# Performance work log

Measured on AMD Instinct MI355X. Metric: run time of the kernel, lower is better.

The kernel has to match this reference:

```python
import jax, jax.numpy as jnp
import numpy as np

B, F, W, H, D = 128, 1024, 32, 64, 64  # batch, n_features, window_size, hidden_state, output_dim


def setup_inputs() -> dict:
    key = jax.random.key(0)
    ks = jax.random.split(key, 8)
    sd = 0.05
    return {
        "x": jax.random.normal(ks[0], (B, F, W), jnp.float32),
        # dense_state: Dense(output_dim) on concat([cell, hidden]) -> [2H, D]
        "W_state": jax.random.normal(ks[1], (2 * H, D), jnp.float32) * sd,
        "b_state": jnp.zeros((D,), jnp.float32),
        # dense: Dense(output_dim, use_bias=False) on input last dim W -> [W, D]
        "W_in": jax.random.normal(ks[2], (W, D), jnp.float32) * sd,
        # Dense(1) scoring layer (shared; original re-creates it each call)
        "w_attn": jax.random.normal(ks[3], (D, 1), jnp.float32) * sd,
        "b_attn": jnp.zeros((1,), jnp.float32),
        # Keras LSTMCell params, gate order i, f, g(c~), o
        "Wx": jax.random.normal(ks[4], (F, 4 * H), jnp.float32) * sd,
        "Wh": jax.random.normal(ks[5], (H, 4 * H), jnp.float32) * sd,
        "b_lstm": jnp.zeros((4 * H,), jnp.float32),
    }


def _forward(x, W_state, b_state, W_in, w_attn, b_attn, Wx, Wh, b_lstm):
    b, f, w = x.shape
    h_dim = Wh.shape[0]
    # dense(input) is loop-invariant: [B, F, D]
    dense_in = jnp.einsum('bfw,wd->bfd', x, W_in)
    xs = jnp.moveaxis(x, 2, 0)  # [W, B, F]: per-timestep slices input[:, :, i]
    h0 = jnp.zeros((b, h_dim), x.dtype)
    c0 = jnp.zeros((b, h_dim), x.dtype)

    def step(carry, x_t):
        h, c = carry
        # original unpacks `s, h = state` with state=[h,c], so it concats [cell, hidden]
        attn_in = jnp.concatenate([c, h], axis=1)             # [B, 2H]
        z = jnp.tanh(attn_in @ W_state + b_state)[:, None, :] + dense_in  # [B, F, D]
        presoft = z @ w_attn + b_attn                         # [B, F, 1]
        # faithful: softmax over last (size-1) axis -> all ones
        alpha = jax.nn.softmax(presoft, axis=-1)
        x_tilde = alpha[..., 0] * x_t                         # [B, F]
        gates = x_tilde @ Wx + h @ Wh + b_lstm                # [B, 4H]
        i_g, f_g, g_g, o_g = jnp.split(gates, 4, axis=1)
        c_new = jax.nn.sigmoid(f_g) * c + jax.nn.sigmoid(i_g) * jnp.tanh(g_g)
        h_new = jax.nn.sigmoid(o_g) * jnp.tanh(c_new)
        # original appends state[1] == CELL state (due to the s,h swap)
        return (h_new, c_new), c_new

    _, outs = jax.lax.scan(step, (h0, c0), xs)                # [W, B, H]
    return jnp.transpose(outs, (1, 0, 2))                     # [B, W, H]


def reference(x, W_state, b_state, W_in, w_attn, b_attn, Wx, Wh, b_lstm):
    return _forward(x, W_state, b_state, W_in, w_attn, b_attn, Wx, Wh, b_lstm)
```

## Files before the change

### kernel.cpp

```cpp
#include <hip/hip_runtime.h>
#include <math.h>

#define B_   128
#define F_   1024
#define W_   32
#define H_   64
#define K4H  256

__global__ __launch_bounds__(256) void gates_gemm(
    const float* __restrict__ x,
    const float* __restrict__ Wx,
    float* __restrict__ G) {
  __shared__ float As[32][64];
  __shared__ float Bs[32][64];

  const int tid   = threadIdx.x;
  const int tm    = tid & 15;
  const int tn    = tid >> 4;
  const int mtile = blockIdx.x;
  const int ntile = blockIdx.y;
  const int b0    = mtile * 2;

  float acc[4][4];
#pragma unroll
  for (int i = 0; i < 4; ++i)
#pragma unroll
    for (int j = 0; j < 4; ++j) acc[i][j] = 0.f;

  for (int f0 = 0; f0 < F_; f0 += 32) {
#pragma unroll
    for (int i = 0; i < 2; ++i) {
      int l  = tid + i * 256;
      int t0 = (l & 7) * 4;
      int fl = (l >> 3) & 31;
      int bl = l >> 8;
      float4 v = *(const float4*)&x[(((size_t)(b0 + bl)) * F_ + (f0 + fl)) * W_ + t0];
      *(float4*)&As[fl][bl * 32 + t0] = v;
    }
#pragma unroll
    for (int i = 0; i < 2; ++i) {
      int l  = tid + i * 256;
      int n0 = (l & 15) * 4;
      int fl = l >> 4;
      float4 v = *(const float4*)&Wx[(size_t)(f0 + fl) * K4H + ntile * 64 + n0];
      *(float4*)&Bs[fl][n0] = v;
    }
    __syncthreads();

#pragma unroll
    for (int f = 0; f < 32; ++f) {
      float4 a4 = *(const float4*)&As[f][tm * 4];
      float4 b4 = *(const float4*)&Bs[f][tn * 4];
      float av[4] = {a4.x, a4.y, a4.z, a4.w};
      float bv[4] = {b4.x, b4.y, b4.z, b4.w};
#pragma unroll
      for (int i = 0; i < 4; ++i)
#pragma unroll
        for (int j = 0; j < 4; ++j)
          acc[i][j] = fmaf(av[i], bv[j], acc[i][j]);
    }
    __syncthreads();
  }

#pragma unroll
  for (int i = 0; i < 4; ++i) {
    int m = mtile * 64 + tm * 4 + i;
    int k = ntile * 64 + tn * 4;
    float4 v = make_float4(acc[i][0], acc[i][1], acc[i][2], acc[i][3]);
    *(float4*)&G[(size_t)m * K4H + k] = v;
  }
}

__device__ __forceinline__ float fast_sigmoid(float v) {
  return 1.f / (1.f + __expf(-v));
}
__device__ __forceinline__ float fast_tanh(float v) {
  return 1.f - 2.f / (__expf(2.f * v) + 1.f);
}

__global__ __launch_bounds__(256) void lstm_seq(
    const float* __restrict__ G,
    const float* __restrict__ Wh,
    const float* __restrict__ bl,
    float* __restrict__ out) {
  __shared__ float sh[H_];
  __shared__ float sact[K4H];

  const int b = blockIdx.x;
  const int k = threadIdx.x;

  float wcol[H_];
#pragma unroll
  for (int j = 0; j < H_; ++j) wcol[j] = Wh[j * K4H + k];
  const float bias = bl[k];

  float c = 0.f;
  if (k < H_) sh[k] = 0.f;
  __syncthreads();

  const float* Gb = G + (size_t)b * W_ * K4H;
  float* outb = out + (size_t)b * W_ * H_;

  for (int t = 0; t < W_; ++t) {
    float g = Gb[t * K4H + k] + bias;
#pragma unroll
    for (int j = 0; j < H_; ++j) g = fmaf(sh[j], wcol[j], g);

    float act;
    if (k < 2 * H_ || k >= 3 * H_) {
      act = fast_sigmoid(g);
    } else {
      act = fast_tanh(g);
    }
    sact[k] = act;
    __syncthreads();

    if (k < H_) {
      float ig = sact[k];
      float fg = sact[H_ + k];
      float gg = sact[2 * H_ + k];
      float og = sact[3 * H_ + k];
      c = fg * c + ig * gg;
      sh[k] = og * fast_tanh(c);
      outb[t * H_ + k] = c;
    }
    __syncthreads();
  }
}

extern "C" void kernel_launch(void* const* d_in, const int* in_sizes, int n_in,
                              void* d_out, int out_size, void* d_ws, size_t ws_size,
                              hipStream_t stream) {
  const float* x      = (const float*)d_in[0];
  const float* Wx     = (const float*)d_in[6];
  const float* Wh     = (const float*)d_in[7];
  const float* b_lstm = (const float*)d_in[8];
  float* out = (float*)d_out;
  float* G   = (float*)d_ws;

  dim3 g1(64, 4);
  gates_gemm<<<g1, dim3(256), 0, stream>>>(x, Wx, G);
  lstm_seq<<<dim3(B_), dim3(256), 0, stream>>>(G, Wh, b_lstm, out);
}
```

Baseline: 147.0 us.

## Use split-bf16 MFMA GEMM with split-K and a register-broadcast LSTM recurrence

```diff
diff --git a/kernel.cpp b/kernel.cpp
--- a/kernel.cpp
+++ b/kernel.cpp
@@ -6,125 +6,221 @@
 #define W_   32
 #define H_   64
 #define K4H  256
-
-__global__ __launch_bounds__(256) void gates_gemm(
+#define M_   (B_ * W_)
+#define K2_  (2 * F_)
+
+typedef __attribute__((ext_vector_type(8))) short  short8;
+typedef __attribute__((ext_vector_type(4))) float  f32x4;
+
+__device__ __forceinline__ unsigned bf16_rne(float v) {
+  unsigned u = __float_as_uint(v);
+  return (u + 0x7FFFu + ((u >> 16) & 1u)) >> 16;
+}
+__device__ __forceinline__ unsigned pack_hilo(float v) {
+  unsigned hi = bf16_rne(v);
+  float    hf = __uint_as_float(hi << 16);
+  unsigned lo = bf16_rne(v - hf);
+  return hi | (lo << 16);
+}
+
+__global__ __launch_bounds__(256) void conv_w(const float* __restrict__ Wx,
+                                              unsigned* __restrict__ B2) {
+  __shared__ unsigned T[256][17];
+  const int tid = threadIdx.x;
+  const int f0  = blockIdx.x * 16;
+#pragma unroll
+  for (int i = 0; i < 4; ++i) {
+    int l = tid + i * 256;
+    int n0 = (l & 63) * 4;
+    int fl = l >> 6;
+    float4 v = *(const float4*)&Wx[(size_t)(f0 + fl) * K4H + n0];
+    T[n0 + 0][fl] = pack_hilo(v.x);
+    T[n0 + 1][fl] = pack_hilo(v.y);
+    T[n0 + 2][fl] = pack_hilo(v.z);
+    T[n0 + 3][fl] = pack_hilo(v.w);
+  }
+  __syncthreads();
+#pragma unroll
+  for (int i = 0; i < 4; ++i) {
+    int l  = tid + i * 256;
+    int c4 = (l & 3) * 4;
+    int n  = l >> 2;
+    uint4 o;
+    o.x = T[n][c4 + 0]; o.y = T[n][c4 + 1]; o.z = T[n][c4 + 2]; o.w = T[n][c4 + 3];
+    *(uint4*)&B2[(size_t)n * (K2_ / 2) + f0 + c4] = o;
+  }
+}
+
+__global__ __launch_bounds__(256) void gemm_mfma(
     const float* __restrict__ x,
-    const float* __restrict__ Wx,
-    float* __restrict__ G) {
-  __shared__ float As[32][64];
-  __shared__ float Bs[32][64];
-
+    const unsigned* __restrict__ B2,
+    float* __restrict__ Gp, int S) {
+  __shared__ unsigned lA[128 * 36];
+  __shared__ unsigned lB[128 * 36];
   const int tid   = threadIdx.x;
-  const int tm    = tid & 15;
-  const int tn    = tid >> 4;
   const int mtile = blockIdx.x;
   const int ntile = blockIdx.y;
-  const int b0    = mtile * 2;
-
-  float acc[4][4];
-#pragma unroll
-  for (int i = 0; i < 4; ++i)
-#pragma unroll
-    for (int j = 0; j < 4; ++j) acc[i][j] = 0.f;
-
-  for (int f0 = 0; f0 < F_; f0 += 32) {
-#pragma unroll
-    for (int i = 0; i < 2; ++i) {
+  const int s     = blockIdx.z;
+  const int NIT   = 32 / S;
+  const int wv = tid >> 6, lane = tid & 63;
+  const int wm = wv & 1, wn = wv >> 1;
+  const int lm = lane & 15, q = lane >> 4;
+
+  f32x4 acc[4][4];
+#pragma unroll
+  for (int a = 0; a < 4; ++a)
+#pragma unroll
+    for (int bb = 0; bb < 4; ++bb) acc[a][bb] = (f32x4){0.f, 0.f, 0.f, 0.f};
+
+  const int b0 = mtile * 4;
+  float4 ax[4];
+  uint4  bxr[4];
+
+  auto prefetch = [&](int iter) {
+    const int f0 = (s * NIT + iter) * 32;
+#pragma unroll
+    for (int i = 0; i < 4; ++i) {
       int l  = tid + i * 256;
       int t0 = (l & 7) * 4;
       int fl = (l >> 3) & 31;
       int bl = l >> 8;
-      float4 v = *(const float4*)&x[(((size_t)(b0 + bl)) * F_ + (f0 + fl)) * W_ + t0];
-      *(float4*)&As[fl][bl * 32 + t0] = v;
-    }
-#pragma unroll
-    for (int i = 0; i < 2; ++i) {
+      ax[i] = *(const float4*)&x[(((size_t)(b0 + bl)) * F_ + (f0 + fl)) * W_ + t0];
+    }
+#pragma unroll
+    for (int i = 0; i < 4; ++i) {
+      int l   = tid + i * 256;
+      int c16 = l & 7;
+      int nl  = l >> 3;
+      bxr[i] = *(const uint4*)&B2[(size_t)(ntile * 128 + nl) * (K2_ / 2) + f0 + c16 * 4];
+    }
+  };
+
+  prefetch(0);
+  for (int iter = 0; iter < NIT; ++iter) {
+    __syncthreads();
+#pragma unroll
+    for (int i = 0; i < 4; ++i) {
       int l  = tid + i * 256;
-      int n0 = (l & 15) * 4;
-      int fl = l >> 4;
-      float4 v = *(const float4*)&Wx[(size_t)(f0 + fl) * K4H + ntile * 64 + n0];
-      *(float4*)&Bs[fl][n0] = v;
+      int t0 = (l & 7) * 4;
+      int fl = (l >> 3) & 31;
+      int bl = l >> 8;
+      int m  = bl * 32 + t0;
+      lA[(m + 0) * 36 + fl] = pack_hilo(ax[i].x);
+      lA[(m + 1) * 36 + fl] = pack_hilo(ax[i].y);
+      lA[(m + 2) * 36 + fl] = pack_hilo(ax[i].z);
+      lA[(m + 3) * 36 + fl] = pack_hilo(ax[i].w);
+    }
+#pragma unroll
+    for (int i = 0; i < 4; ++i) {
+      int l   = tid + i * 256;
+      int c16 = l & 7;
+      int nl  = l >> 3;
+      *(uint4*)&lB[nl * 36 + c16 * 4] = bxr[i];
     }
     __syncthreads();
-
-#pragma unroll
-    for (int f = 0; f < 32; ++f) {
-      float4 a4 = *(const float4*)&As[f][tm * 4];
-      float4 b4 = *(const float4*)&Bs[f][tn * 4];
-      float av[4] = {a4.x, a4.y, a4.z, a4.w};
-      float bv[4] = {b4.x, b4.y, b4.z, b4.w};
-#pragma unroll
-      for (int i = 0; i < 4; ++i)
-#pragma unroll
-        for (int j = 0; j < 4; ++j)
-          acc[i][j] = fmaf(av[i], bv[j], acc[i][j]);
-    }
+    if (iter + 1 < NIT) prefetch(iter + 1);
+#pragma unroll
+    for (int step = 0; step < 2; ++step) {
+      short8 aF[4], bF[4];
+#pragma unroll
+      for (int mt = 0; mt < 4; ++mt) {
+        int row = wm * 64 + mt * 16 + lm;
+        aF[mt] = *(const short8*)&lA[row * 36 + step * 16 + q * 4];
+      }
+#pragma unroll
+      for (int nt = 0; nt < 4; ++nt) {
+        int row = wn * 64 + nt * 16 + lm;
+        bF[nt] = *(const short8*)&lB[row * 36 + step * 16 + q * 4];
+      }
+#pragma unroll
+      for (int mt = 0; mt < 4; ++mt)
+#pragma unroll
+        for (int nt = 0; nt < 4; ++nt)
+          acc[mt][nt] = __builtin_amdgcn_mfma_f32_16x16x32_bf16(
+              aF[mt], bF[nt], acc[mt][nt], 0, 0, 0);
+    }
+  }
+  float* Gs = Gp + (size_t)s * ((size_t)M_ * K4H);
+#pragma unroll
+  for (int mt = 0; mt < 4; ++mt)
+#pragma unroll
+    for (int nt = 0; nt < 4; ++nt)
+#pragma unroll
+      for (int r = 0; r < 4; ++r) {
+        int m = mtile * 128 + wm * 64 + mt * 16 + q * 4 + r;
+        int n = ntile * 128 + wn * 64 + nt * 16 + lm;
+        Gs[(size_t)m * K4H + n] = acc[mt][nt][r];
+      }
+}
+
+__device__ __forceinline__ float bcastlane(float v, int l) {
+  return __uint_as_float(__builtin_amdgcn_readlane(__float_as_uint(v), l));
+}
+__device__ __forceinline__ float sigm(float v)  { return 1.f / (1.f + __expf(-v)); }
+__device__ __forceinline__ float tanh_f(float v){ return 1.f - 2.f / (__expf(2.f * v) + 1.f); }
+
+__global__ __launch_bounds__(128) void lstm_seq(
+    const float* __restrict__ Gp, const float* __restrict__ Wh,
+    const float* __restrict__ bl, float* __restrict__ out, int S) {
+  __shared__ float2 ex[2][2][64];
+  const int b = blockIdx.x, tid = threadIdx.x;
+  const int w = tid >> 6, u = tid & 63;
+  const int kA = w * 128 + u, kB = kA + 64;
+
+  float wA[64], wB[64];
+#pragma unroll
+  for (int j = 0; j < 64; ++j) {
+    wA[j] = Wh[j * K4H + kA];
+    wB[j] = Wh[j * K4H + kB];
+  }
+  const float bA = bl[kA], bB = bl[kB];
+  const size_t base = (size_t)b * W_ * K4H;
+  const size_t sstr = (size_t)M_ * K4H;
+
+  float h = 0.f, c = 0.f;
+  float cA[4] = {0, 0, 0, 0}, cB[4] = {0, 0, 0, 0};
+  for (int ss = 0; ss < S; ++ss) {
+    cA[ss] = Gp[ss * sstr + base + kA];
+    cB[ss] = Gp[ss * sstr + base + kB];
+  }
+  for (int t = 0; t < W_; ++t) {
+    float nA[4] = {0, 0, 0, 0}, nB[4] = {0, 0, 0, 0};
+    if (t + 1 < W_) {
+      for (int ss = 0; ss < S; ++ss) {
+        nA[ss] = Gp[ss * sstr + base + (t + 1) * K4H + kA];
+        nB[ss] = Gp[ss * sstr + base + (t + 1) * K4H + kB];
+      }
+    }
+    float gA = bA + ((cA[0] + cA[1]) + (cA[2] + cA[3]));
+    float gB = bB + ((cB[0] + cB[1]) + (cB[2] + cB[3]));
+    float a0 = gA, a1 = 0, a2 = 0, a3 = 0;
+    float e0 = gB, e1 = 0, e2 = 0, e3 = 0;
+#pragma unroll
+    for (int j = 0; j < 64; j += 4) {
+      float h0 = bcastlane(h, j),     h1 = bcastlane(h, j + 1);
+      float h2 = bcastlane(h, j + 2), h3 = bcastlane(h, j + 3);
+      a0 = fmaf(h0, wA[j],     a0);  e0 = fmaf(h0, wB[j],     e0);
+      a1 = fmaf(h1, wA[j + 1], a1);  e1 = fmaf(h1, wB[j + 1], e1);
+      a2 = fmaf(h2, wA[j + 2], a2);  e2 = fmaf(h2, wB[j + 2], e2);
+      a3 = fmaf(h3, wA[j + 3], a3);  e3 = fmaf(h3, wB[j + 3], e3);
+    }
+    gA = (a0 + a1) + (a2 + a3);
+    gB = (e0 + e1) + (e2 + e3);
+    float eA, eB;
+    if (w == 0) { eA = sigm(gA);   eB = sigm(gB); }
+    else        { eA = tanh_f(gA); eB = sigm(gB); }
+    ex[t & 1][w][u] = make_float2(eA, eB);
     __syncthreads();
-  }
-
-#pragma unroll
-  for (int i = 0; i < 4; ++i) {
-    int m = mtile * 64 + tm * 4 + i;
-    int k = ntile * 64 + tn * 4;
-    float4 v = make_float4(acc[i][0], acc[i][1], acc[i][2], acc[i][3]);
-    *(float4*)&G[(size_t)m * K4H + k] = v;
-  }
-}
-
-__device__ __forceinline__ float fast_sigmoid(float v) {
-  return 1.f / (1.f + __expf(-v));
-}
-__device__ __forceinline__ float fast_tanh(float v) {
-  return 1.f - 2.f / (__expf(2.f * v) + 1.f);
-}
-
-__global__ __launch_bounds__(256) void lstm_seq(
-    const float* __restrict__ G,
-    const float* __restrict__ Wh,
-    const float* __restrict__ bl,
-    float* __restrict__ out) {
-  __shared__ float sh[H_];
-  __shared__ float sact[K4H];
-
-  const int b = blockIdx.x;
-  const int k = threadIdx.x;
-
-  float wcol[H_];
-#pragma unroll
-  for (int j = 0; j < H_; ++j) wcol[j] = Wh[j * K4H + k];
-  const float bias = bl[k];
-
-  float c = 0.f;
-  if (k < H_) sh[k] = 0.f;
-  __syncthreads();
-
-  const float* Gb = G + (size_t)b * W_ * K4H;
-  float* outb = out + (size_t)b * W_ * H_;
-
-  for (int t = 0; t < W_; ++t) {
-    float g = Gb[t * K4H + k] + bias;
-#pragma unroll
-    for (int j = 0; j < H_; ++j) g = fmaf(sh[j], wcol[j], g);
-
-    float act;
-    if (k < 2 * H_ || k >= 3 * H_) {
-      act = fast_sigmoid(g);
-    } else {
-      act = fast_tanh(g);
-    }
-    sact[k] = act;
-    __syncthreads();
-
-    if (k < H_) {
-      float ig = sact[k];
-      float fg = sact[H_ + k];
-      float gg = sact[2 * H_ + k];
-      float og = sact[3 * H_ + k];
-      c = fg * c + ig * gg;
-      sh[k] = og * fast_tanh(c);
-      outb[t * H_ + k] = c;
-    }
-    __syncthreads();
+    float2 o = ex[t & 1][1 - w][u];
+    float si = (w == 0) ? eA : o.x;
+    float sf = (w == 0) ? eB : o.y;
+    float tg = (w == 0) ? o.x : eA;
+    float so = (w == 0) ? o.y : eB;
+    c = fmaf(sf, c, si * tg);
+    h = so * tanh_f(c);
+    if (w == 0) out[((size_t)b * W_ + t) * H_ + u] = c;
+#pragma unroll
+    for (int ss = 0; ss < 4; ++ss) { cA[ss] = nA[ss]; cB[ss] = nB[ss]; }
   }
 }
 
@@ -136,9 +232,16 @@
   const float* Wh     = (const float*)d_in[7];
   const float* b_lstm = (const float*)d_in[8];
   float* out = (float*)d_out;
-  float* G   = (float*)d_ws;
-
-  dim3 g1(64, 4);
-  gates_gemm<<<g1, dim3(256), 0, stream>>>(x, Wx, G);
-  lstm_seq<<<dim3(B_), dim3(256), 0, stream>>>(G, Wh, b_lstm, out);
-}
+
+  const size_t gbytes = (size_t)M_ * K4H * sizeof(float);
+  int S;
+  if      (ws_size >= 4 * gbytes + (1u << 20)) S = 4;
+  else if (ws_size >= 2 * gbytes + (1u << 20)) S = 2;
+  else                                         S = 1;
+  float*    Gp = (float*)d_ws;
+  unsigned* B2 = (unsigned*)((char*)d_ws + (size_t)S * gbytes);
+
+  conv_w  <<<dim3(64),        dim3(256), 0, stream>>>(Wx, B2);
+  gemm_mfma<<<dim3(32, 2, S), dim3(256), 0, stream>>>(x, B2, Gp, S);
+  lstm_seq<<<dim3(B_),        dim3(128), 0, stream>>>(Gp, Wh, b_lstm, out, S);
+}
```

New measurement: 152.8 us. +4.0%, slower.
